# Optimization experiments

Hardware: AMD Instinct MI355X
Metric: run time of the kernel (lower is better)

The kernel has to match this reference:

```python
import jax, jax.numpy as jnp
import numpy as np

N = 50000
E = 800000
IN_C = 128
HID = 64
NUM_LAYERS = 3
OUT_C = 1


def _lin_params(key, fan_in, fan_out, bias=True):
    k1, k2 = jax.random.split(key)
    s = 1.0 / np.sqrt(fan_in)
    W = jax.random.uniform(k1, (fan_out, fan_in), jnp.float32, -s, s)
    b = jax.random.uniform(k2, (fan_out,), jnp.float32, -s, s) if bias else None
    return W, b


def setup_inputs() -> dict:
    key = jax.random.key(0)
    ks = jax.random.split(key, 16)
    x = jax.random.normal(ks[0], (N, IN_C), jnp.float32)
    src = jax.random.randint(ks[1], (E,), 0, N, jnp.int32)
    dst = jax.random.randint(ks[2], (E,), 0, N, jnp.int32)
    inp = {"x": x, "src": src, "dst": dst}
    # SAGEConv layers: lin_l (neighbors, with bias), lin_r (root, no bias)
    dims = [(IN_C, HID)] + [(HID, HID)] * (NUM_LAYERS - 1)
    for i, (fi, fo) in enumerate(dims):
        Wl, bl = _lin_params(ks[3 + 2 * i], fi, fo, bias=True)
        Wr, _ = _lin_params(ks[4 + 2 * i], fi, fo, bias=False)
        inp[f"Wl{i}"] = Wl
        inp[f"bl{i}"] = bl
        inp[f"Wr{i}"] = Wr
    node_emb = HID * NUM_LAYERS
    Wm1, bm1 = _lin_params(ks[10], 2 * node_emb, HID, bias=True)
    Wm2, bm2 = _lin_params(ks[11], HID, OUT_C, bias=True)
    inp.update(Wm1=Wm1, bm1=bm1, Wm2=Wm2, bm2=bm2)
    return inp


def _sage(x, src, dst, Wl, bl, Wr):
    # mean-aggregate neighbor features at dst (message flows src -> dst)
    msg_sum = jax.ops.segment_sum(x[src], dst, num_segments=N)  # [N, F]
    deg = jax.ops.segment_sum(jnp.ones((src.shape[0], 1), x.dtype), dst,
                              num_segments=N)  # [N, 1]
    agg = msg_sum / jnp.maximum(deg, 1.0)
    return agg @ Wl.T + bl + x @ Wr.T


def reference(x, src, dst, Wl0, bl0, Wr0, Wl1, bl1, Wr1, Wl2, bl2, Wr2,
              Wm1, bm1, Wm2, bm2):
    layers = [(Wl0, bl0, Wr0), (Wl1, bl1, Wr1), (Wl2, bl2, Wr2)]
    outs = []
    h = x
    for Wl, bl, Wr in layers:
        h = jax.nn.relu(_sage(h, src, dst, Wl, bl, Wr))
        outs.append(h)
    x_cat = jnp.concatenate(outs, axis=-1)  # [N, HID*NUM_LAYERS]
    edge_repr = jnp.concatenate([x_cat[src], x_cat[dst]], axis=-1)  # [E, 2*node_emb]
    hidden = jax.nn.relu(edge_repr @ Wm1.T + bm1)
    edge_pred = hidden @ Wm2.T + bm2  # [E, 1]
    return edge_pred.squeeze(-1)
```

## Files before the change

### kernel.cpp

```cpp
#include <hip/hip_runtime.h>

#define N_NODES 50000
#define N_EDGES 800000
#define IN_CH   128
#define HID     64
#define SCAN_BLOCKS ((N_NODES + 255) / 256)
#define NXCD 8
#define NODES_PER_XCD (N_NODES / NXCD)

typedef __attribute__((ext_vector_type(8))) short bf16x8;
typedef __attribute__((ext_vector_type(4))) float f32x4;


__device__ inline float bfraw(unsigned int bits) {
  float f; __builtin_memcpy(&f, &bits, 4); return f;
}
__device__ inline float bf2f(unsigned short u) {
  return bfraw(((unsigned int)u) << 16);
}
__device__ inline unsigned short f2bf(float f) {
  unsigned int x; __builtin_memcpy(&x, &f, 4);
  return (unsigned short)((x + 0x7FFFu + ((x >> 16) & 1u)) >> 16);
}


__global__ __launch_bounds__(256) void k_count_slot(const int* __restrict__ dst,
                                                    int* __restrict__ deg,
                                                    int* __restrict__ slot) {
  int e = blockIdx.x * 256 + threadIdx.x;
  if (e < N_EDGES) slot[e] = atomicAdd(&deg[dst[e]], 1);
}

__global__ __launch_bounds__(256) void k_blocksum(const int* __restrict__ deg,
                                                  int* __restrict__ bsum) {
  int t = threadIdx.x, lane = t & 63, wid = t >> 6;
  int i = blockIdx.x * 256 + t;
  int v = (i < N_NODES) ? deg[i] : 0;
#pragma unroll
  for (int d = 32; d > 0; d >>= 1) v += __shfl_down(v, d);
  __shared__ int ws[4];
  if (lane == 0) ws[wid] = v;
  __syncthreads();
  if (t == 0) bsum[blockIdx.x] = ws[0] + ws[1] + ws[2] + ws[3];
}

__global__ __launch_bounds__(256) void k_scanb(const int* __restrict__ bsum,
                                               int* __restrict__ boff,
                                               int* __restrict__ rowstart) {
  int t = threadIdx.x, lane = t & 63, wid = t >> 6;
  int v = (t < SCAN_BLOCKS) ? bsum[t] : 0;
  int orig = v;
#pragma unroll
  for (int d = 1; d < 64; d <<= 1) {
    int u = __shfl_up(v, d);
    if (lane >= d) v += u;
  }
  __shared__ int ws[4];
  if (lane == 63) ws[wid] = v;
  __syncthreads();
  int off = 0;
  for (int j = 0; j < wid; ++j) off += ws[j];
  if (t < SCAN_BLOCKS) boff[t] = v - orig + off;
  if (t == 0) rowstart[N_NODES] = N_EDGES;
}

__global__ __launch_bounds__(256) void k_local(const int* __restrict__ deg,
                                               const int* __restrict__ boff,
                                               int* __restrict__ rowstart) {
  int t = threadIdx.x, lane = t & 63, wid = t >> 6;
  int i = blockIdx.x * 256 + t;
  int orig = (i < N_NODES) ? deg[i] : 0;
  int v = orig;
#pragma unroll
  for (int d = 1; d < 64; d <<= 1) {
    int u = __shfl_up(v, d);
    if (lane >= d) v += u;
  }
  __shared__ int ws[4];
  if (lane == 63) ws[wid] = v;
  __syncthreads();
  int off = boff[blockIdx.x];
  for (int j = 0; j < wid; ++j) off += ws[j];
  if (i < N_NODES) rowstart[i] = v - orig + off;
}

__global__ __launch_bounds__(256) void k_abs(const int* __restrict__ dst,
                                             const int* __restrict__ rowstart,
                                             int* __restrict__ slot) {
  int e = blockIdx.x * 256 + threadIdx.x;
  if (e < N_EDGES) slot[e] = rowstart[dst[e]] + slot[e];
}

__global__ __launch_bounds__(256) void k_place(const int* __restrict__ src,
                                               const int* __restrict__ slot,
                                               const int* __restrict__ rowstart,
                                               int2* __restrict__ csr_pack) {
  int xcd = blockIdx.x & (NXCD - 1);
  int e = (blockIdx.x >> 3) * 256 + threadIdx.x;
  int lo = rowstart[xcd * NODES_PER_XCD];
  int hi = rowstart[(xcd + 1) * NODES_PER_XCD];
  if (e < N_EDGES) {
    int sl = slot[e];
    if (sl >= lo && sl < hi) csr_pack[sl] = make_int2(src[e], e);
  }
}


__global__ __launch_bounds__(256) void conv_x(const float* __restrict__ x,
                                              unsigned short* __restrict__ xh,
                                              unsigned short* __restrict__ xl) {
  size_t base = ((size_t)blockIdx.x * 256 + threadIdx.x) * 8;
  float4 a = *(const float4*)&x[base];
  float4 b = *(const float4*)&x[base + 4];
  float v[8] = {a.x, a.y, a.z, a.w, b.x, b.y, b.z, b.w};
  unsigned short h[8], l[8];
#pragma unroll
  for (int j = 0; j < 8; ++j) {
    h[j] = f2bf(v[j]);
    l[j] = f2bf(v[j] - bf2f(h[j]));
  }
  uint4 uh = make_uint4((unsigned)h[0] | ((unsigned)h[1] << 16),
                        (unsigned)h[2] | ((unsigned)h[3] << 16),
                        (unsigned)h[4] | ((unsigned)h[5] << 16),
                        (unsigned)h[6] | ((unsigned)h[7] << 16));
  uint4 ul = make_uint4((unsigned)l[0] | ((unsigned)l[1] << 16),
                        (unsigned)l[2] | ((unsigned)l[3] << 16),
                        (unsigned)l[4] | ((unsigned)l[5] << 16),
                        (unsigned)l[6] | ((unsigned)l[7] << 16));
  *(uint4*)&xh[base] = uh;
  *(uint4*)&xl[base] = ul;
}

__global__ __launch_bounds__(256) void convW(const float* __restrict__ Wa,
                                             const float* __restrict__ Wb, int ldW, int K,
                                             unsigned short* __restrict__ Bh,
                                             unsigned short* __restrict__ Bl) {
  int r = blockIdx.x;
  int k = threadIdx.x;
  const float* wsrc = (r < 64) ? (Wa + (size_t)r * ldW) : (Wb + (size_t)(r - 64) * ldW);
  float v = wsrc[k];
  unsigned short hi = f2bf(v);
  Bh[(size_t)r * K + k] = hi;
  Bl[(size_t)r * K + k] = f2bf(v - bf2f(hi));
}


__global__ __launch_bounds__(256)
void gemm_mfma(const unsigned short* __restrict__ Ah, const unsigned short* __restrict__ Al,
               int ldA, int K,
               const unsigned short* __restrict__ Bh, const unsigned short* __restrict__ Bl,
               const float* __restrict__ bias,
               unsigned short* __restrict__ outA, float* __restrict__ outB) {
  int t = threadIdx.x;
  int lane = t & 63, wave = t >> 6;
  int r0 = blockIdx.x * 64;
  int col0 = wave * 32;
  int lrow = lane & 15;
  int kgrp = (lane >> 4) * 8;

  f32x4 z = {0.f, 0.f, 0.f, 0.f};
  f32x4 acc[4][2];
#pragma unroll
  for (int rt = 0; rt < 4; ++rt)
#pragma unroll
    for (int ct = 0; ct < 2; ++ct) acc[rt][ct] = z;

  int arow[4];
#pragma unroll
  for (int rt = 0; rt < 4; ++rt) {
    int r = r0 + rt * 16 + lrow;
    arow[rt] = (r < N_NODES) ? r : (N_NODES - 1);
  }
  int bcol0 = col0 + lrow;

  for (int k0 = 0; k0 < K; k0 += 32) {
    bf16x8 ah[4], al[4], bh[2], bl[2];
#pragma unroll
    for (int rt = 0; rt < 4; ++rt) {
      size_t o = (size_t)arow[rt] * ldA + k0 + kgrp;
      ah[rt] = *(const bf16x8*)(Ah + o);
      al[rt] = *(const bf16x8*)(Al + o);
    }
#pragma unroll
    for (int ct = 0; ct < 2; ++ct) {
      size_t o = (size_t)(bcol0 + ct * 16) * K + k0 + kgrp;
      bh[ct] = *(const bf16x8*)(Bh + o);
      bl[ct] = *(const bf16x8*)(Bl + o);
    }
#pragma unroll
    for (int rt = 0; rt < 4; ++rt)
#pragma unroll
      for (int ct = 0; ct < 2; ++ct) {
        acc[rt][ct] = __builtin_amdgcn_mfma_f32_16x16x32_bf16(ah[rt], bh[ct], acc[rt][ct], 0, 0, 0);
        acc[rt][ct] = __builtin_amdgcn_mfma_f32_16x16x32_bf16(al[rt], bh[ct], acc[rt][ct], 0, 0, 0);
        acc[rt][ct] = __builtin_amdgcn_mfma_f32_16x16x32_bf16(ah[rt], bl[ct], acc[rt][ct], 0, 0, 0);
      }
  }

  int crow = (lane >> 4) * 4;
#pragma unroll
  for (int ct = 0; ct < 2; ++ct) {
    int col = col0 + ct * 16 + lrow;
    bool isA = (col < 64);
    float bv = 0.f;
    if (!isA) bv = bias[col - 64];
#pragma unroll
    for (int rt = 0; rt < 4; ++rt) {
#pragma unroll
      for (int reg = 0; reg < 4; ++reg) {
        int row = r0 + rt * 16 + crow + reg;
        if (row < N_NODES) {
          float v = acc[rt][ct][reg];
          if (isA) outA[(size_t)row * 64 + col] = f2bf(v);
          else     outB[(size_t)row * 64 + (col - 64)] = v + bv;
        }
      }
    }
  }
}


__global__ __launch_bounds__(256)
void agg_fuse(const unsigned short* __restrict__ y_nb, const float* __restrict__ y_rt,
              const int* __restrict__ rowstart, const int2* __restrict__ csr_pack,
              unsigned short* __restrict__ oh, unsigned short* __restrict__ ol) {
  int w = (blockIdx.x * 256 + threadIdx.x) >> 6;
  int lane = threadIdx.x & 63;
  if (w >= N_NODES) return;
  int beg = rowstart[w], end = rowstart[w + 1];
  int cnt = end - beg;
  int grp = lane >> 3;
  int l8  = lane & 7;
  float s0 = 0.f, s1 = 0.f, s2 = 0.f, s3 = 0.f;
  float s4 = 0.f, s5 = 0.f, s6 = 0.f, s7 = 0.f;

  int i = 0;
  for (; i + 16 <= cnt; i += 16) {
    int na = csr_pack[beg + i + grp].x;
    int nb = csr_pack[beg + i + 8 + grp].x;
    uint4 a = *(const uint4*)&y_nb[(size_t)na * 64 + l8 * 8];
    uint4 b = *(const uint4*)&y_nb[(size_t)nb * 64 + l8 * 8];
    s0 += bfraw(a.x << 16);  s1 += bfraw(a.x & 0xFFFF0000u);
    s2 += bfraw(a.y << 16);  s3 += bfraw(a.y & 0xFFFF0000u);
    s4 += bfraw(a.z << 16);  s5 += bfraw(a.z & 0xFFFF0000u);
    s6 += bfraw(a.w << 16);  s7 += bfraw(a.w & 0xFFFF0000u);
    s0 += bfraw(b.x << 16);  s1 += bfraw(b.x & 0xFFFF0000u);
    s2 += bfraw(b.y << 16);  s3 += bfraw(b.y & 0xFFFF0000u);
    s4 += bfraw(b.z << 16);  s5 += bfraw(b.z & 0xFFFF0000u);
    s6 += bfraw(b.w << 16);  s7 += bfraw(b.w & 0xFFFF0000u);
  }
  for (; i + 8 <= cnt; i += 8) {
    int na = csr_pack[beg + i + grp].x;
    uint4 a = *(const uint4*)&y_nb[(size_t)na * 64 + l8 * 8];
    s0 += bfraw(a.x << 16);  s1 += bfraw(a.x & 0xFFFF0000u);
    s2 += bfraw(a.y << 16);  s3 += bfraw(a.y & 0xFFFF0000u);
    s4 += bfraw(a.z << 16);  s5 += bfraw(a.z & 0xFFFF0000u);
    s6 += bfraw(a.w << 16);  s7 += bfraw(a.w & 0xFFFF0000u);
  }
  int rem = cnt - i;
  if (grp < rem) {
    int na = csr_pack[beg + i + grp].x;
    uint4 a = *(const uint4*)&y_nb[(size_t)na * 64 + l8 * 8];
    s0 += bfraw(a.x << 16);  s1 += bfraw(a.x & 0xFFFF0000u);
    s2 += bfraw(a.y << 16);  s3 += bfraw(a.y & 0xFFFF0000u);
    s4 += bfraw(a.z << 16);  s5 += bfraw(a.z & 0xFFFF0000u);
    s6 += bfraw(a.w << 16);  s7 += bfraw(a.w & 0xFFFF0000u);
  }

  s0 += __shfl_xor(s0, 8); s0 += __shfl_xor(s0, 16); s0 += __shfl_xor(s0, 32);
  s1 += __shfl_xor(s1, 8); s1 += __shfl_xor(s1, 16); s1 += __shfl_xor(s1, 32);
  s2 += __shfl_xor(s2, 8); s2 += __shfl_xor(s2, 16); s2 += __shfl_xor(s2, 32);
  s3 += __shfl_xor(s3, 8); s3 += __shfl_xor(s3, 16); s3 += __shfl_xor(s3, 32);
  s4 += __shfl_xor(s4, 8); s4 += __shfl_xor(s4, 16); s4 += __shfl_xor(s4, 32);
  s5 += __shfl_xor(s5, 8); s5 += __shfl_xor(s5, 16); s5 += __shfl_xor(s5, 32);
  s6 += __shfl_xor(s6, 8); s6 += __shfl_xor(s6, 16); s6 += __shfl_xor(s6, 32);
  s7 += __shfl_xor(s7, 8); s7 += __shfl_xor(s7, 16); s7 += __shfl_xor(s7, 32);

  if (grp == 0) {
    float inv = 1.0f / fmaxf((float)cnt, 1.0f);
    const float* rt = &y_rt[(size_t)w * 64 + l8 * 8];
    float4 ra = *(const float4*)rt;
    float4 rb = *(const float4*)(rt + 4);
    float h0 = fmaxf(s0 * inv + ra.x, 0.f);
    float h1 = fmaxf(s1 * inv + ra.y, 0.f);
    float h2 = fmaxf(s2 * inv + ra.z, 0.f);
    float h3 = fmaxf(s3 * inv + ra.w, 0.f);
    float h4 = fmaxf(s4 * inv + rb.x, 0.f);
    float h5 = fmaxf(s5 * inv + rb.y, 0.f);
    float h6 = fmaxf(s6 * inv + rb.z, 0.f);
    float h7 = fmaxf(s7 * inv + rb.w, 0.f);
    unsigned short i0 = f2bf(h0), i1 = f2bf(h1), i2 = f2bf(h2), i3 = f2bf(h3);
    unsigned short i4 = f2bf(h4), i5 = f2bf(h5), i6 = f2bf(h6), i7 = f2bf(h7);
    uint4 ph = make_uint4((unsigned)i0 | ((unsigned)i1 << 16),
                          (unsigned)i2 | ((unsigned)i3 << 16),
                          (unsigned)i4 | ((unsigned)i5 << 16),
                          (unsigned)i6 | ((unsigned)i7 << 16));
    unsigned short j0 = f2bf(h0 - bf2f(i0)), j1 = f2bf(h1 - bf2f(i1));
    unsigned short j2 = f2bf(h2 - bf2f(i2)), j3 = f2bf(h3 - bf2f(i3));
    unsigned short j4 = f2bf(h4 - bf2f(i4)), j5 = f2bf(h5 - bf2f(i5));
    unsigned short j6 = f2bf(h6 - bf2f(i6)), j7 = f2bf(h7 - bf2f(i7));
    uint4 pl = make_uint4((unsigned)j0 | ((unsigned)j1 << 16),
                          (unsigned)j2 | ((unsigned)j3 << 16),
                          (unsigned)j4 | ((unsigned)j5 << 16),
                          (unsigned)j6 | ((unsigned)j7 << 16));
    *(uint4*)&oh[(size_t)w * 192 + l8 * 8] = ph;
    *(uint4*)&ol[(size_t)w * 192 + l8 * 8] = pl;
  }
}


__global__ __launch_bounds__(256)
void edge_mlp_csr(const int* __restrict__ rowstart, const int2* __restrict__ csr_pack,
                  const unsigned short* __restrict__ Pb, const float* __restrict__ Qf,
                  const float* __restrict__ wm2, const float* __restrict__ bm2v,
                  float* __restrict__ out) {
  int wv = (blockIdx.x * 256 + threadIdx.x) >> 6;
  if (wv >= N_NODES) return;
  int lane = threadIdx.x & 63;
  int grp = lane >> 3, l8 = lane & 7;
  int beg = rowstart[wv], end = rowstart[wv + 1];
  if (beg == end) return;
  const float* qp = &Qf[(size_t)wv * 64 + l8 * 8];
  float4 qa = *(const float4*)qp;
  float4 qb = *(const float4*)(qp + 4);
  float4 wa = *(const float4*)&wm2[l8 * 8];
  float4 wb = *(const float4*)&wm2[l8 * 8 + 4];
  float b2 = bm2v[0];
  for (int i = beg + grp; i < end; i += 8) {
    int2 pk = csr_pack[i];
    int s = pk.x;
    int eid = pk.y;
    uint4 pu = *(const uint4*)&Pb[(size_t)s * 64 + l8 * 8];
    float p0 = bfraw(pu.x << 16), p1 = bfraw(pu.x & 0xFFFF0000u);
    float p2 = bfraw(pu.y << 16), p3 = bfraw(pu.y & 0xFFFF0000u);
    float p4 = bfraw(pu.z << 16), p5 = bfraw(pu.z & 0xFFFF0000u);
    float p6 = bfraw(pu.w << 16), p7 = bfraw(pu.w & 0xFFFF0000u);
    float part = fmaxf(p0 + qa.x, 0.f) * wa.x
               + fmaxf(p1 + qa.y, 0.f) * wa.y
               + fmaxf(p2 + qa.z, 0.f) * wa.z
               + fmaxf(p3 + qa.w, 0.f) * wa.w
               + fmaxf(p4 + qb.x, 0.f) * wb.x
               + fmaxf(p5 + qb.y, 0.f) * wb.y
               + fmaxf(p6 + qb.z, 0.f) * wb.z
               + fmaxf(p7 + qb.w, 0.f) * wb.w;
    part += __shfl_xor(part, 1);
    part += __shfl_xor(part, 2);
    part += __shfl_xor(part, 4);
    if (l8 == 0) out[eid] = part + b2;
  }
}


extern "C" void kernel_launch(void* const* d_in, const int* in_sizes, int n_in,
                              void* d_out, int out_size, void* d_ws, size_t ws_size,
                              hipStream_t stream) {
  (void)in_sizes; (void)n_in; (void)out_size; (void)ws_size;
  const float* x   = (const float*)d_in[0];
  const int*   src = (const int*)d_in[1];
  const int*   dst = (const int*)d_in[2];
  const float* Wl0 = (const float*)d_in[3];
  const float* bl0 = (const float*)d_in[4];
  const float* Wr0 = (const float*)d_in[5];
  const float* Wl1 = (const float*)d_in[6];
  const float* bl1 = (const float*)d_in[7];
  const float* Wr1 = (const float*)d_in[8];
  const float* Wl2 = (const float*)d_in[9];
  const float* bl2 = (const float*)d_in[10];
  const float* Wr2 = (const float*)d_in[11];
  const float* Wm1 = (const float*)d_in[12];
  const float* bm1 = (const float*)d_in[13];
  const float* Wm2 = (const float*)d_in[14];
  const float* bm2 = (const float*)d_in[15];
  float* out = (float*)d_out;

  char* ws = (char*)d_ws;
  size_t off = 0;
  auto take = [&](size_t bytes) {
    char* p = ws + off;
    off = (off + bytes + 255) & ~(size_t)255;
    return p;
  };
  int*   deg      = (int*)take((size_t)N_NODES * 4);
  int*   rowstart = (int*)take((size_t)(N_NODES + 1) * 4);
  int*   bsum     = (int*)take((size_t)SCAN_BLOCKS * 4);
  int*   boff     = (int*)take((size_t)SCAN_BLOCKS * 4);
  int2*  csr_pack = (int2*)take((size_t)N_EDGES * 8);
  unsigned short* xh = (unsigned short*)take((size_t)N_NODES * 192 * 2);
  unsigned short* xl = (unsigned short*)take((size_t)N_NODES * 192 * 2);
  unsigned short* y_nb = (unsigned short*)take((size_t)N_NODES * 64 * 2);
  float* y_rt     = (float*)take((size_t)N_NODES * 64 * 4);
  unsigned short* W0h = (unsigned short*)take((size_t)128 * 192 * 2);
  unsigned short* W0l = (unsigned short*)take((size_t)128 * 192 * 2);
  unsigned short* W1h = (unsigned short*)take((size_t)128 * 192 * 2);
  unsigned short* W1l = (unsigned short*)take((size_t)128 * 192 * 2);
  unsigned short* W2h = (unsigned short*)take((size_t)128 * 192 * 2);
  unsigned short* W2l = (unsigned short*)take((size_t)128 * 192 * 2);
  unsigned short* Wmh = (unsigned short*)take((size_t)128 * 192 * 2);
  unsigned short* Wml = (unsigned short*)take((size_t)128 * 192 * 2);
  int* slot = (int*)y_rt;

  hipMemsetAsync(deg, 0, (size_t)N_NODES * 4, stream);

  int edge_grid = (N_EDGES + 255) / 256;
  k_count_slot<<<edge_grid, 256, 0, stream>>>(dst, deg, slot);
  k_blocksum<<<SCAN_BLOCKS, 256, 0, stream>>>(deg, bsum);
  k_scanb<<<1, 256, 0, stream>>>(bsum, boff, rowstart);
  k_local<<<SCAN_BLOCKS, 256, 0, stream>>>(deg, boff, rowstart);
  k_abs<<<edge_grid, 256, 0, stream>>>(dst, rowstart, slot);
  k_place<<<edge_grid * NXCD, 256, 0, stream>>>(src, slot, rowstart, csr_pack);

  conv_x<<<(N_NODES * IN_CH / 8 + 255) / 256, 256, 0, stream>>>(x, xh, xl);
  convW<<<128, 128, 0, stream>>>(Wl0, Wr0, IN_CH, 128, W0h, W0l);
  convW<<<128,  64, 0, stream>>>(Wl1, Wr1, HID,   64, W1h, W1l);
  convW<<<128,  64, 0, stream>>>(Wl2, Wr2, HID,   64, W2h, W2l);
  convW<<<128, 192, 0, stream>>>(Wm1, Wm1 + 192, 384, 192, Wmh, Wml);

  int gemm_grid = (N_NODES + 63) / 64;
  int node_waves_grid = (N_NODES * 64) / 256;
  gemm_mfma<<<gemm_grid, 256, 0, stream>>>(xh, xl, 128, 128, W0h, W0l, bl0, y_nb, y_rt);
  agg_fuse<<<node_waves_grid, 256, 0, stream>>>(y_nb, y_rt, rowstart, csr_pack, xh + 0, xl + 0);
  gemm_mfma<<<gemm_grid, 256, 0, stream>>>(xh, xl, 192, 64, W1h, W1l, bl1, y_nb, y_rt);
  agg_fuse<<<node_waves_grid, 256, 0, stream>>>(y_nb, y_rt, rowstart, csr_pack, xh + 64, xl + 64);
  gemm_mfma<<<gemm_grid, 256, 0, stream>>>(xh + 64, xl + 64, 192, 64, W2h, W2l, bl2, y_nb, y_rt);
  agg_fuse<<<node_waves_grid, 256, 0, stream>>>(y_nb, y_rt, rowstart, csr_pack, xh + 128, xl + 128);
  gemm_mfma<<<gemm_grid, 256, 0, stream>>>(xh, xl, 192, 192, Wmh, Wml, bm1, y_nb, y_rt);
  edge_mlp_csr<<<node_waves_grid, 256, 0, stream>>>(rowstart, csr_pack, y_nb, y_rt, Wm2, bm2, out);
}
```

Measured before the change: 298.9 us.

## Store activations and weights in MFMA-fragment panel layout for coalesced GEMM loads

Activations (hi/lo bf16 split) and weights are now written in a 16-row panel layout where each 32-wide K slice for 16 rows is contiguous, so each wave's fragment load becomes one fully coalesced 1 KB read instead of 16 strided row segments. The GEMM is templated on K so the K loop fully unrolls with constant offsets. The conversion and aggregation kernels scatter their outputs into this layout, which makes those stores less contiguous per row. The GEMM loads are meant to get cheaper in exchange.

Result: faster. 260.1 us (-13.0%).

```diff
diff --git a/kernel.cpp b/kernel.cpp
--- a/kernel.cpp
+++ b/kernel.cpp
@@ -7,6 +7,8 @@
 #define SCAN_BLOCKS ((N_NODES + 255) / 256)
 #define NXCD 8
 #define NODES_PER_XCD (N_NODES / NXCD)
+#define NPANEL (N_NODES / 16)
+#define PSTR   3072
 
 typedef __attribute__((ext_vector_type(8))) short bf16x8;
 typedef __attribute__((ext_vector_type(4))) float f32x4;
@@ -107,11 +109,13 @@
 
 
 __global__ __launch_bounds__(256) void conv_x(const float* __restrict__ x,
-                                              unsigned short* __restrict__ xh,
-                                              unsigned short* __restrict__ xl) {
-  size_t base = ((size_t)blockIdx.x * 256 + threadIdx.x) * 8;
-  float4 a = *(const float4*)&x[base];
-  float4 b = *(const float4*)&x[base + 4];
+                                              unsigned short* __restrict__ xch,
+                                              unsigned short* __restrict__ xcl) {
+  int idx = blockIdx.x * 256 + threadIdx.x;
+  int n = idx >> 4, kc = idx & 15;
+  const float* p = x + (size_t)n * 128 + kc * 8;
+  float4 a = *(const float4*)p;
+  float4 b = *(const float4*)(p + 4);
   float v[8] = {a.x, a.y, a.z, a.w, b.x, b.y, b.z, b.w};
   unsigned short h[8], l[8];
 #pragma unroll
@@ -127,8 +131,9 @@
                         (unsigned)l[2] | ((unsigned)l[3] << 16),
                         (unsigned)l[4] | ((unsigned)l[5] << 16),
                         (unsigned)l[6] | ((unsigned)l[7] << 16));
-  *(uint4*)&xh[base] = uh;
-  *(uint4*)&xl[base] = ul;
+  size_t o = (size_t)(n >> 4) * PSTR + kc * 128 + (n & 15) * 8;
+  *(uint4*)&xch[o] = uh;
+  *(uint4*)&xcl[o] = ul;
 }
 
 __global__ __launch_bounds__(256) void convW(const float* __restrict__ Wa,
@@ -140,14 +145,15 @@
   const float* wsrc = (r < 64) ? (Wa + (size_t)r * ldW) : (Wb + (size_t)(r - 64) * ldW);
   float v = wsrc[k];
   unsigned short hi = f2bf(v);
-  Bh[(size_t)r * K + k] = hi;
-  Bl[(size_t)r * K + k] = f2bf(v - bf2f(hi));
-}
-
-
+  size_t o = (size_t)(r >> 4) * ((size_t)K * 16) + (k >> 3) * 128 + (r & 15) * 8 + (k & 7);
+  Bh[o] = hi;
+  Bl[o] = f2bf(v - bf2f(hi));
+}
+
+
+template<int K>
 __global__ __launch_bounds__(256)
 void gemm_mfma(const unsigned short* __restrict__ Ah, const unsigned short* __restrict__ Al,
-               int ldA, int K,
                const unsigned short* __restrict__ Bh, const unsigned short* __restrict__ Bl,
                const float* __restrict__ bias,
                unsigned short* __restrict__ outA, float* __restrict__ outB) {
@@ -156,7 +162,6 @@
   int r0 = blockIdx.x * 64;
   int col0 = wave * 32;
   int lrow = lane & 15;
-  int kgrp = (lane >> 4) * 8;
 
   f32x4 z = {0.f, 0.f, 0.f, 0.f};
   f32x4 acc[4][2];
@@ -165,25 +170,31 @@
 #pragma unroll
     for (int ct = 0; ct < 2; ++ct) acc[rt][ct] = z;
 
-  int arow[4];
+  size_t abase[4];
 #pragma unroll
   for (int rt = 0; rt < 4; ++rt) {
-    int r = r0 + rt * 16 + lrow;
-    arow[rt] = (r < N_NODES) ? r : (N_NODES - 1);
-  }
-  int bcol0 = col0 + lrow;
-
-  for (int k0 = 0; k0 < K; k0 += 32) {
+    int p = blockIdx.x * 4 + rt;
+    if (p > NPANEL - 1) p = NPANEL - 1;
+    abase[rt] = (size_t)p * PSTR + (size_t)lane * 8;
+  }
+  size_t bbase[2];
+#pragma unroll
+  for (int ct = 0; ct < 2; ++ct)
+    bbase[ct] = (size_t)(wave * 2 + ct) * ((size_t)K * 16) + (size_t)lane * 8;
+
+  constexpr int NK = K / 32;
+#pragma unroll
+  for (int ks = 0; ks < NK; ++ks) {
     bf16x8 ah[4], al[4], bh[2], bl[2];
 #pragma unroll
     for (int rt = 0; rt < 4; ++rt) {
-      size_t o = (size_t)arow[rt] * ldA + k0 + kgrp;
+      size_t o = abase[rt] + ks * 512;
       ah[rt] = *(const bf16x8*)(Ah + o);
       al[rt] = *(const bf16x8*)(Al + o);
     }
 #pragma unroll
     for (int ct = 0; ct < 2; ++ct) {
-      size_t o = (size_t)(bcol0 + ct * 16) * K + k0 + kgrp;
+      size_t o = bbase[ct] + ks * 512;
       bh[ct] = *(const bf16x8*)(Bh + o);
       bl[ct] = *(const bf16x8*)(Bl + o);
     }
@@ -223,7 +234,8 @@
 __global__ __launch_bounds__(256)
 void agg_fuse(const unsigned short* __restrict__ y_nb, const float* __restrict__ y_rt,
               const int* __restrict__ rowstart, const int2* __restrict__ csr_pack,
-              unsigned short* __restrict__ oh, unsigned short* __restrict__ ol) {
+              unsigned short* __restrict__ oh, unsigned short* __restrict__ ol,
+              int coff_e) {
   int w = (blockIdx.x * 256 + threadIdx.x) >> 6;
   int lane = threadIdx.x & 63;
   if (w >= N_NODES) return;
@@ -303,8 +315,9 @@
                           (unsigned)j2 | ((unsigned)j3 << 16),
                           (unsigned)j4 | ((unsigned)j5 << 16),
                           (unsigned)j6 | ((unsigned)j7 << 16));
-    *(uint4*)&oh[(size_t)w * 192 + l8 * 8] = ph;
-    *(uint4*)&ol[(size_t)w * 192 + l8 * 8] = pl;
+    size_t o = (size_t)(w >> 4) * PSTR + coff_e + l8 * 128 + (w & 15) * 8;
+    *(uint4*)&oh[o] = ph;
+    *(uint4*)&ol[o] = pl;
   }
 }
 
@@ -385,8 +398,8 @@
   int*   bsum     = (int*)take((size_t)SCAN_BLOCKS * 4);
   int*   boff     = (int*)take((size_t)SCAN_BLOCKS * 4);
   int2*  csr_pack = (int2*)take((size_t)N_EDGES * 8);
-  unsigned short* xh = (unsigned short*)take((size_t)N_NODES * 192 * 2);
-  unsigned short* xl = (unsigned short*)take((size_t)N_NODES * 192 * 2);
+  unsigned short* xch = (unsigned short*)take((size_t)NPANEL * PSTR * 2);
+  unsigned short* xcl = (unsigned short*)take((size_t)NPANEL * PSTR * 2);
   unsigned short* y_nb = (unsigned short*)take((size_t)N_NODES * 64 * 2);
   float* y_rt     = (float*)take((size_t)N_NODES * 64 * 4);
   unsigned short* W0h = (unsigned short*)take((size_t)128 * 192 * 2);
@@ -409,7 +422,7 @@
   k_abs<<<edge_grid, 256, 0, stream>>>(dst, rowstart, slot);
   k_place<<<edge_grid * NXCD, 256, 0, stream>>>(src, slot, rowstart, csr_pack);
 
-  conv_x<<<(N_NODES * IN_CH / 8 + 255) / 256, 256, 0, stream>>>(x, xh, xl);
+  conv_x<<<(N_NODES * 16) / 256, 256, 0, stream>>>(x, xch, xcl);
   convW<<<128, 128, 0, stream>>>(Wl0, Wr0, IN_CH, 128, W0h, W0l);
   convW<<<128,  64, 0, stream>>>(Wl1, Wr1, HID,   64, W1h, W1l);
   convW<<<128,  64, 0, stream>>>(Wl2, Wr2, HID,   64, W2h, W2l);
@@ -417,12 +430,12 @@
 
   int gemm_grid = (N_NODES + 63) / 64;
   int node_waves_grid = (N_NODES * 64) / 256;
-  gemm_mfma<<<gemm_grid, 256, 0, stream>>>(xh, xl, 128, 128, W0h, W0l, bl0, y_nb, y_rt);
-  agg_fuse<<<node_waves_grid, 256, 0, stream>>>(y_nb, y_rt, rowstart, csr_pack, xh + 0, xl + 0);
-  gemm_mfma<<<gemm_grid, 256, 0, stream>>>(xh, xl, 192, 64, W1h, W1l, bl1, y_nb, y_rt);
-  agg_fuse<<<node_waves_grid, 256, 0, stream>>>(y_nb, y_rt, rowstart, csr_pack, xh + 64, xl + 64);
-  gemm_mfma<<<gemm_grid, 256, 0, stream>>>(xh + 64, xl + 64, 192, 64, W2h, W2l, bl2, y_nb, y_rt);
-  agg_fuse<<<node_waves_grid, 256, 0, stream>>>(y_nb, y_rt, rowstart, csr_pack, xh + 128, xl + 128);
-  gemm_mfma<<<gemm_grid, 256, 0, stream>>>(xh, xl, 192, 192, Wmh, Wml, bm1, y_nb, y_rt);
+  gemm_mfma<128><<<gemm_grid, 256, 0, stream>>>(xch, xcl, W0h, W0l, bl0, y_nb, y_rt);
+  agg_fuse<<<node_waves_grid, 256, 0, stream>>>(y_nb, y_rt, rowstart, csr_pack, xch, xcl, 0);
+  gemm_mfma<64><<<gemm_grid, 256, 0, stream>>>(xch, xcl, W1h, W1l, bl1, y_nb, y_rt);
+  agg_fuse<<<node_waves_grid, 256, 0, stream>>>(y_nb, y_rt, rowstart, csr_pack, xch, xcl, 1024);
+  gemm_mfma<64><<<gemm_grid, 256, 0, stream>>>(xch + 1024, xcl + 1024, W2h, W2l, bl2, y_nb, y_rt);
+  agg_fuse<<<node_waves_grid, 256, 0, stream>>>(y_nb, y_rt, rowstart, csr_pack, xch, xcl, 2048);
+  gemm_mfma<192><<<gemm_grid, 256, 0, stream>>>(xch, xcl, Wmh, Wml, bm1, y_nb, y_rt);
   edge_mlp_csr<<<node_waves_grid, 256, 0, stream>>>(rowstart, csr_pack, y_nb, y_rt, Wm2, bm2, out);
 }
```
